# Kernel optimization log

Measured on AMD Instinct MI355X. Metric: run time of the kernel, lower is better.

## Reference

```python
import jax, jax.numpy as jnp
import numpy as np

# config (mirrors init_kwargs)
H = 768        # hidden_size
NH = 12        # n_heads
HD = H // NH   # head_size = 64 (rotary 'per_head' dim)
INTER = 3072   # intermediate_size
NL = 6         # n_layers
V = 32768      # vocab_size
AW = 256       # attention_width
SEQLEN = 512   # packed per-sequence length (batch['length'])
B = 16         # number of packed sequences
N = B * SEQLEN # total tokens


def _layer_norm(x, scale, offset, eps=1e-5):
    m = jnp.mean(x, axis=-1, keepdims=True)
    var = jnp.mean(jnp.square(x - m), axis=-1, keepdims=True)
    return (x - m) * jax.lax.rsqrt(var + eps) * scale + offset


def _rotate_every_two(x):
    x1 = x[..., ::2]
    x2 = x[..., 1::2]
    return jnp.stack((-x2, x1), axis=-1).reshape(x.shape)


def _fixed_pos_embedding(ages, dim):
    # ages: [N] float32 -> sin, cos: [N, dim]
    inv_freq = 1.0 / 10000 ** jnp.linspace(0.0, 2.0, num=dim // 2)
    t = ages[:, None] * inv_freq[None, :]          # [N, dim//2]
    s, c = jnp.sin(t), jnp.cos(t)
    sin = jnp.stack((s, s), axis=-1).reshape(ages.shape[0], dim)
    cos = jnp.stack((c, c), axis=-1).reshape(ages.shape[0], dim)
    return sin, cos


def _local_attention(q, k, v, seg_len, width):
    # q,k,v: [NH, N, HD]. Causal attention within a sliding window of `width`,
    # restricted to segments of size seg_len (the (i & ~(length-1)) mask in piton).
    nh, n, hd = q.shape
    b = n // seg_len
    qb = q.reshape(nh, b, seg_len, hd)
    kb = k.reshape(nh, b, seg_len, hd)
    vb = v.reshape(nh, b, seg_len, hd)
    scale = jnp.asarray(1.0 / np.sqrt(hd), q.dtype)
    scores = jnp.einsum('hbqd,hbkd->hbqk', qb, kb) * scale
    i = jnp.arange(seg_len)[:, None]
    j = jnp.arange(seg_len)[None, :]
    mask = (j <= i) & (i - j < width)
    scores = jnp.where(mask, scores, jnp.asarray(-1e30, scores.dtype))
    probs = jax.nn.softmax(scores, axis=-1)
    out = jnp.einsum('hbqk,hbkd->hbqd', probs, vb)
    return out.reshape(nh, n, hd)


def _block(x, sin, cos, seg_len, p):
    scale, offset, w_in, b_in, w_out, b_out = p
    xn = _layer_norm(x, scale, offset)
    mid = xn @ w_in + b_in                               # fused QKV + FF proj
    q, k, v, ff = jnp.split(mid, [H, 2 * H, 3 * H], axis=-1)

    def to_heads(t):  # [N, H] -> [NH, N, HD]
        return t.reshape(t.shape[0], NH, HD).transpose(1, 0, 2)

    q, k, v = to_heads(q), to_heads(k), to_heads(v)
    # rotary == 'per_head': applied after head split, sin/cos broadcast over heads
    q = q * cos[None] + _rotate_every_two(q) * sin[None]
    k = k * cos[None] + _rotate_every_two(k) * sin[None]
    attn = _local_attention(q, k, v, seg_len, AW)
    shaped = attn.transpose(1, 0, 2).reshape(x.shape)    # [N, H]
    combined = jnp.concatenate((shaped, jax.nn.gelu(ff)), axis=-1)
    # NOTE: original returns normed-x + output_proj(combined) (x was reassigned)
    return xn + combined @ w_out + b_out


def setup_inputs() -> dict:
    key = jax.random.key(0)
    ks = jax.random.split(key, 8)
    return {
        'tokens': jax.random.randint(ks[0], (N,), 0, V, dtype=jnp.int32),
        'ages': jax.random.uniform(ks[1], (N,), jnp.float32, 0.0, 10000.0),
        'normalized_ages': jax.random.normal(ks[2], (N,), jnp.float32),
        'length': SEQLEN,
        'embed': jax.random.normal(ks[3], (V, H), jnp.float32) / np.sqrt(H),
        'ln_scale': jnp.ones((NL, H), jnp.float32),
        'ln_offset': jnp.zeros((NL, H), jnp.float32),
        'w_in': jax.random.normal(ks[4], (NL, H, 3 * H + INTER), jnp.float32) / np.sqrt(H),
        'b_in': jnp.zeros((NL, 3 * H + INTER), jnp.float32),
        'w_out': jax.random.normal(ks[5], (NL, H + INTER, H), jnp.float32) * (2.0 / (NL * np.sqrt(H))),
        'b_out': jnp.zeros((NL, H), jnp.float32),
        'final_scale': jnp.ones((H,), jnp.float32),
        'final_offset': jnp.zeros((H,), jnp.float32),
    }


def reference(tokens, ages, normalized_ages, length, embed, ln_scale, ln_offset,
              w_in, b_in, w_out, b_out, final_scale, final_offset):
    x = embed[tokens]                                  # [N, H]
    sin, cos = _fixed_pos_embedding(ages, HD)          # rotary == 'per_head'

    def step(carry, p):
        return _block(carry, sin, cos, length, p), None

    x, _ = jax.lax.scan(step, x, (ln_scale, ln_offset, w_in, b_in, w_out, b_out))
    return _layer_norm(x, final_scale, final_offset)
```

## Files before the change

### kernel.cpp

```cpp
#include <hip/hip_runtime.h>
#include <hip/hip_bf16.h>

#define H_    768
#define NH_   12
#define HD_   64
#define INTER_ 3072
#define NL_   6
#define NTOK  8192
#define SEG   512
#define NB    16
#define AW_   256
#define MIDW  5376
#define CMB   3840

typedef unsigned short u16;
typedef __bf16 bf16;
typedef bf16  bf16x8 __attribute__((ext_vector_type(8)));
typedef float f32x4  __attribute__((ext_vector_type(4)));
typedef u16   u16x8  __attribute__((ext_vector_type(8)));

#define GLOAD16(gp, lp) \
    __builtin_amdgcn_global_load_lds((const __attribute__((address_space(1))) void*)(gp), \
                                     (__attribute__((address_space(3))) void*)(lp), 16, 0, 0)

__device__ __forceinline__ u16 f2bf(float f) {
    union { float f; unsigned u; } v; v.f = f;
    unsigned u = v.u;
    u += 0x7fffu + ((u >> 16) & 1u);
    return (u16)(u >> 16);
}
__device__ __forceinline__ float bf2f(u16 h) {
    union { unsigned u; float f; } v; v.u = ((unsigned)h) << 16; return v.f;
}
__device__ __forceinline__ float gelu_f(float x) {
    float x3 = x * x * x;
    return 0.5f * x * (1.f + tanhf(0.7978845608028654f * (x + 0.044715f * x3)));
}

__global__ void k_embed(const int* __restrict__ tokens, const float* __restrict__ embed,
                        float* __restrict__ x) {
    int row = blockIdx.x;
    int tok = tokens[row];
    const float* src = embed + (size_t)tok * H_;
    float* dst = x + (size_t)row * H_;
    for (int c = threadIdx.x; c < H_; c += blockDim.x) dst[c] = src[c];
}

__global__ void k_tables(const float* __restrict__ ages, float* __restrict__ st,
                         float* __restrict__ ct) {
    int n = blockIdx.x * blockDim.x + threadIdx.x;
    if (n >= NTOK) return;
    float age = ages[n];
    for (int j = 0; j < 32; j++) {
        float e = (float)j * (2.0f / 31.0f);
        float invf = 1.0f / powf(10000.0f, e);
        float t = age * invf;
        st[n * 32 + j] = sinf(t);
        ct[n * 32 + j] = cosf(t);
    }
}

__global__ void k_transpose_bf16(const float* __restrict__ src, u16* __restrict__ dst,
                                 int R, int C) {
    __shared__ float T[64][65];
    int l = blockIdx.z;
    const float* s = src + (size_t)l * R * C;
    u16* d = dst + (size_t)l * R * C;
    int r0 = blockIdx.y * 64, c0 = blockIdx.x * 64;
    for (int i = threadIdx.x; i < 64 * 64; i += blockDim.x) {
        int r = i >> 6, c = i & 63;
        T[r][c] = s[(size_t)(r0 + r) * C + c0 + c];
    }
    __syncthreads();
    for (int i = threadIdx.x; i < 64 * 64; i += blockDim.x) {
        int rr = i >> 6, cc = i & 63;
        d[(size_t)(c0 + rr) * R + r0 + cc] = f2bf(T[cc][rr]);
    }
}

template<int FINAL>
__global__ __launch_bounds__(256) void k_ln(const float* __restrict__ x,
        const float* __restrict__ scale, const float* __restrict__ offset,
        float* __restrict__ xn_f, u16* __restrict__ xn_h, float* __restrict__ outf) {
    int wid = threadIdx.x >> 6, lane = threadIdx.x & 63;
    int row = blockIdx.x * 4 + wid;
    const float* xr = x + (size_t)row * H_;
    float4 v[3];
    float s = 0.f, sq = 0.f;
#pragma unroll
    for (int i = 0; i < 3; i++) {
        v[i] = *(const float4*)&xr[(i * 64 + lane) * 4];
        s  += v[i].x + v[i].y + v[i].z + v[i].w;
        sq += v[i].x * v[i].x + v[i].y * v[i].y + v[i].z * v[i].z + v[i].w * v[i].w;
    }
    for (int m = 1; m < 64; m <<= 1) { s += __shfl_xor(s, m); sq += __shfl_xor(sq, m); }
    float mean = s * (1.f / 768.f);
    float var  = sq * (1.f / 768.f) - mean * mean;
    float rstd = rsqrtf(fmaxf(var, 0.f) + 1e-5f);
#pragma unroll
    for (int i = 0; i < 3; i++) {
        int c0 = (i * 64 + lane) * 4;
        float4 sc = *(const float4*)&scale[c0];
        float4 of = *(const float4*)&offset[c0];
        float y0 = (v[i].x - mean) * rstd * sc.x + of.x;
        float y1 = (v[i].y - mean) * rstd * sc.y + of.y;
        float y2 = (v[i].z - mean) * rstd * sc.z + of.z;
        float y3 = (v[i].w - mean) * rstd * sc.w + of.w;
        if (FINAL) {
            *(float4*)&outf[(size_t)row * H_ + c0] = make_float4(y0, y1, y2, y3);
        } else {
            *(float4*)&xn_f[(size_t)row * H_ + c0] = make_float4(y0, y1, y2, y3);
            ushort4 h = make_ushort4(f2bf(y0), f2bf(y1), f2bf(y2), f2bf(y3));
            *(ushort4*)&xn_h[(size_t)row * H_ + c0] = h;
        }
    }
}

template<int MODE, int BN>
__global__ __launch_bounds__(256) void k_gemm(
        const u16* __restrict__ A, const u16* __restrict__ A2,
        const u16* __restrict__ Bt, const float* __restrict__ bias,
        const float* __restrict__ xn_f, u16* __restrict__ Cmid,
        float* __restrict__ Xout, int Ksz) {
    __shared__ __align__(16) u16 As[128 * 64];
    __shared__ __align__(16) u16 Bs[BN * 64];
    int m0 = blockIdx.x * 128;
    int n0 = blockIdx.y * BN;
    int tid = threadIdx.x;
    int wid = tid >> 6, lane = tid & 63;
    constexpr int MI = (BN == 128) ? 4 : 2;
    constexpr int NI = 4;
    int wm = (BN == 128) ? (wid >> 1) : wid;
    int wn = (BN == 128) ? (wid & 1) : 0;
    f32x4 acc[MI][NI] = {};

    int r = tid >> 3;
    int cs = ((tid & 7) ^ ((tid >> 3) & 7)) * 8;
    int wbase = (tid & 192) * 8;

    int lm = lane & 15, lq = lane >> 4, l7 = lane & 7;

    int nkt = Ksz / 64;
    for (int kt = 0; kt < nkt; kt++) {
        int k0 = kt * 64;
        const u16* Ap; int lda, acol;
        if (MODE == 2 && k0 >= H_) { Ap = A2; lda = MIDW; acol = 2304 + (k0 - H_); }
        else                       { Ap = A;  lda = H_;   acol = k0; }
#pragma unroll
        for (int i = 0; i < 4; i++)
            GLOAD16(&Ap[(size_t)(m0 + i * 32 + r) * lda + acol + cs], &As[i * 2048 + wbase]);
#pragma unroll
        for (int i = 0; i < BN / 32; i++)
            GLOAD16(&Bt[(size_t)(n0 + i * 32 + r) * Ksz + k0 + cs], &Bs[i * 2048 + wbase]);
        __syncthreads();
#pragma unroll
        for (int kk = 0; kk < 64; kk += 32) {
            int slot = (((kk >> 3) + lq) ^ l7) * 8;
            bf16x8 af[MI], bfr[NI];
#pragma unroll
            for (int mi = 0; mi < MI; mi++)
                af[mi] = *(const bf16x8*)&As[(wm * (MI * 16) + mi * 16 + lm) * 64 + slot];
#pragma unroll
            for (int ni = 0; ni < NI; ni++)
                bfr[ni] = *(const bf16x8*)&Bs[(wn * 64 + ni * 16 + lm) * 64 + slot];
#pragma unroll
            for (int mi = 0; mi < MI; mi++)
#pragma unroll
                for (int ni = 0; ni < NI; ni++)
                    acc[mi][ni] = __builtin_amdgcn_mfma_f32_16x16x32_bf16(af[mi], bfr[ni], acc[mi][ni], 0, 0, 0);
        }
        __syncthreads();
    }
    int rbase = m0 + wm * (MI * 16), cbase = n0 + wn * 64;
#pragma unroll
    for (int mi = 0; mi < MI; mi++) {
#pragma unroll
        for (int ni = 0; ni < NI; ni++) {
            int col = cbase + ni * 16 + lm;
            float b = bias[col];
#pragma unroll
            for (int rr = 0; rr < 4; rr++) {
                int row = rbase + mi * 16 + lq * 4 + rr;
                float vv = acc[mi][ni][rr] + b;
                if (MODE == 1) {
                    if (col >= 2304) vv = gelu_f(vv);
                    Cmid[(size_t)row * MIDW + col] = f2bf(vv);
                } else {
                    Xout[(size_t)row * H_ + col] = vv + xn_f[(size_t)row * H_ + col];
                }
            }
        }
    }
}

__global__ __launch_bounds__(256) void k_rope_v(u16* __restrict__ mid,
        const float* __restrict__ st, const float* __restrict__ ct, u16* __restrict__ Vt) {
    int nb = blockIdx.x, h = blockIdx.y;
    int n0 = nb * 64;
    __shared__ u16 Vl[64][72];
    int tid = threadIdx.x;
    for (int i = tid; i < 64 * 32; i += 256) {
        int r = i >> 5, j = i & 31;
        int n = n0 + r;
        float s = st[n * 32 + j], c = ct[n * 32 + j];
        size_t base = (size_t)n * MIDW + h * 64 + 2 * j;
        float q0 = bf2f(mid[base]), q1 = bf2f(mid[base + 1]);
        mid[base]     = f2bf(q0 * c - q1 * s);
        mid[base + 1] = f2bf(q1 * c + q0 * s);
        float k0 = bf2f(mid[base + H_]), k1 = bf2f(mid[base + H_ + 1]);
        mid[base + H_]     = f2bf(k0 * c - k1 * s);
        mid[base + H_ + 1] = f2bf(k1 * c + k0 * s);
    }
    for (int i = tid; i < 64 * 64; i += 256) {
        int r = i >> 6, d = i & 63;
        Vl[r][d] = mid[(size_t)(n0 + r) * MIDW + 1536 + h * 64 + d];
    }
    __syncthreads();
    for (int i = tid; i < 64 * 64; i += 256) {
        int d = i >> 6, r = i & 63;
        Vt[(size_t)(h * 64 + d) * NTOK + n0 + r] = Vl[r][d];
    }
}

__global__ __launch_bounds__(128) void k_attn(const u16* __restrict__ mid,
        const u16* __restrict__ Vt, u16* __restrict__ attn_out) {
    int bx = blockIdx.x;
    int h = bx >> 8, rem = bx & 255, b = rem >> 4, qq = rem & 15;
    int t0 = (qq * 32 - 255) >> 6; if (t0 < 0) t0 = 0;
    int tend = qq >> 1;
    int nt = tend - t0 + 1;
    int tid = threadIdx.x, wid = tid >> 6, lane = tid & 63;
    __shared__ float S[32][324];
    __shared__ float rl[32];
    int qrow0 = b * SEG + qq * 32;

    bf16x8 qf[2];
    {
        int r = qrow0 + wid * 16 + (lane & 15);
        const u16* qp = &mid[(size_t)r * MIDW + h * 64];
        qf[0] = *(const bf16x8*)&qp[(lane >> 4) * 8];
        qf[1] = *(const bf16x8*)&qp[32 + (lane >> 4) * 8];
    }
    for (int t = 0; t < nt; t++) {
        int j0 = (t0 + t) * 64;
        f32x4 sa[4] = {};
#pragma unroll
        for (int kf = 0; kf < 2; kf++) {
            bf16x8 kfr[4];
#pragma unroll
            for (int nf = 0; nf < 4; nf++) {
                int key = b * SEG + j0 + nf * 16 + (lane & 15);
                kfr[nf] = *(const bf16x8*)&mid[(size_t)key * MIDW + H_ + h * 64 + kf * 32 + (lane >> 4) * 8];
            }
#pragma unroll
            for (int nf = 0; nf < 4; nf++)
                sa[nf] = __builtin_amdgcn_mfma_f32_16x16x32_bf16(qf[kf], kfr[nf], sa[nf], 0, 0, 0);
        }
#pragma unroll
        for (int nf = 0; nf < 4; nf++) {
            int j = j0 + nf * 16 + (lane & 15);
#pragma unroll
            for (int r = 0; r < 4; r++) {
                int row = wid * 16 + (lane >> 4) * 4 + r;
                int qi = qq * 32 + row;
                bool valid = (j <= qi) && (qi - j < AW_);
                S[row][t * 64 + nf * 16 + (lane & 15)] = valid ? sa[nf][r] * 0.125f : -1e30f;
            }
        }
    }
    __syncthreads();
    {
        int row = tid >> 2, sub = tid & 3;
        int ncol = nt * 64;
        float m = -1e30f;
        for (int c = sub; c < ncol; c += 4) m = fmaxf(m, S[row][c]);
        m = fmaxf(m, __shfl_xor(m, 1)); m = fmaxf(m, __shfl_xor(m, 2));
        float l = 0.f;
        for (int c = sub; c < ncol; c += 4) { float p = __expf(S[row][c] - m); S[row][c] = p; l += p; }
        l += __shfl_xor(l, 1); l += __shfl_xor(l, 2);
        if (sub == 0) rl[row] = 1.f / l;
    }
    __syncthreads();
    f32x4 oacc[4] = {};
    for (int t = 0; t < nt; t++) {
#pragma unroll
        for (int kf = 0; kf < 2; kf++) {
            const float* sp = &S[wid * 16 + (lane & 15)][t * 64 + kf * 32 + (lane >> 4) * 8];
            float4 f1 = *(const float4*)sp;
            float4 f2 = *(const float4*)(sp + 4);
            u16x8 pt;
            pt[0] = f2bf(f1.x); pt[1] = f2bf(f1.y); pt[2] = f2bf(f1.z); pt[3] = f2bf(f1.w);
            pt[4] = f2bf(f2.x); pt[5] = f2bf(f2.y); pt[6] = f2bf(f2.z); pt[7] = f2bf(f2.w);
            bf16x8 pa = __builtin_bit_cast(bf16x8, pt);
#pragma unroll
            for (int nf = 0; nf < 4; nf++) {
                int d = h * 64 + nf * 16 + (lane & 15);
                const u16* vp = &Vt[(size_t)d * NTOK + b * SEG + (t0 + t) * 64 + kf * 32 + (lane >> 4) * 8];
                bf16x8 vb = *(const bf16x8*)vp;
                oacc[nf] = __builtin_amdgcn_mfma_f32_16x16x32_bf16(pa, vb, oacc[nf], 0, 0, 0);
            }
        }
    }
#pragma unroll
    for (int nf = 0; nf < 4; nf++) {
#pragma unroll
        for (int r = 0; r < 4; r++) {
            int row = wid * 16 + (lane >> 4) * 4 + r;
            float sc = rl[row];
            int grow = qrow0 + row;
            attn_out[(size_t)grow * H_ + h * 64 + nf * 16 + (lane & 15)] = f2bf(oacc[nf][r] * sc);
        }
    }
}

extern "C" void kernel_launch(void* const* d_in, const int* in_sizes, int n_in,
                              void* d_out, int out_size, void* d_ws, size_t ws_size,
                              hipStream_t stream) {
    const int*   tokens   = (const int*)d_in[0];
    const float* ages     = (const float*)d_in[1];
    const float* embed    = (const float*)d_in[4];
    const float* ln_scale = (const float*)d_in[5];
    const float* ln_off   = (const float*)d_in[6];
    const float* w_in     = (const float*)d_in[7];
    const float* b_in     = (const float*)d_in[8];
    const float* w_out    = (const float*)d_in[9];
    const float* b_out    = (const float*)d_in[10];
    const float* fscale   = (const float*)d_in[11];
    const float* foff     = (const float*)d_in[12];
    float* out = (float*)d_out;

    char* ws = (char*)d_ws;
    size_t off = 0;
    auto alloc = [&](size_t bytes) { void* p = ws + off; off += (bytes + 255) & ~(size_t)255; return p; };
    float* st      = (float*)alloc((size_t)NTOK * 32 * 4);
    float* ct      = (float*)alloc((size_t)NTOK * 32 * 4);
    float* x       = (float*)alloc((size_t)NTOK * H_ * 4);
    float* xn_f    = (float*)alloc((size_t)NTOK * H_ * 4);
    u16*   xn_h    = (u16*)alloc((size_t)NTOK * H_ * 2);
    u16*   mid     = (u16*)alloc((size_t)NTOK * MIDW * 2);
    u16*   Vt      = (u16*)alloc((size_t)H_ * NTOK * 2);
    u16*   attn    = (u16*)alloc((size_t)NTOK * H_ * 2);
    u16*   w_in_t  = (u16*)alloc((size_t)NL_ * H_ * MIDW * 2);
    u16*   w_out_t = (u16*)alloc((size_t)NL_ * CMB * H_ * 2);

    k_embed<<<NTOK, 256, 0, stream>>>(tokens, embed, x);
    k_tables<<<(NTOK + 255) / 256, 256, 0, stream>>>(ages, st, ct);
    k_transpose_bf16<<<dim3(MIDW / 64, H_ / 64, NL_), 256, 0, stream>>>(w_in, w_in_t, H_, MIDW);
    k_transpose_bf16<<<dim3(H_ / 64, CMB / 64, NL_), 256, 0, stream>>>(w_out, w_out_t, CMB, H_);

    for (int l = 0; l < NL_; l++) {
        k_ln<0><<<NTOK / 4, 256, 0, stream>>>(x, ln_scale + l * H_, ln_off + l * H_, xn_f, xn_h, nullptr);
        k_gemm<1, 128><<<dim3(NTOK / 128, MIDW / 128), 256, 0, stream>>>(
            xn_h, nullptr, w_in_t + (size_t)l * H_ * MIDW, b_in + (size_t)l * MIDW,
            nullptr, mid, nullptr, H_);
        k_rope_v<<<dim3(NTOK / 64, NH_), 256, 0, stream>>>(mid, st, ct, Vt);
        k_attn<<<NH_ * NB * 16, 128, 0, stream>>>(mid, Vt, attn);
        k_gemm<2, 64><<<dim3(NTOK / 128, H_ / 64), 256, 0, stream>>>(
            attn, mid, w_out_t + (size_t)l * CMB * H_, b_out + (size_t)l * H_,
            xn_f, nullptr, x, CMB);
    }
    k_ln<1><<<NTOK / 4, 256, 0, stream>>>(x, fscale, foff, nullptr, nullptr, out);
}
```

Measured before the change: 2.077 ms.

## Replace QKV/FF GEMM with 256x256 eight-wave double-buffered pipelined kernel

The first projection GEMM now uses a 512-thread block computing 256x256 tiles, with double-buffered LDS, global-to-LDS prefetch of the next K tile spread across four compute phases, explicit vmcnt waits, raw barriers and setprio around the MFMA bursts. The tanh-based GELU is replaced with an algebraically equivalent exp form using fast intrinsics. The second GEMM is split into its own specialized kernel without template modes. The aim is more operand reuse per tile and overlap of memory loads with matrix math. In exchange the kernel uses 128 KB of LDS per block and needs many accumulator registers, which may limit occupancy.

```diff
diff --git a/kernel.cpp b/kernel.cpp
--- a/kernel.cpp
+++ b/kernel.cpp
@@ -23,6 +23,9 @@
     __builtin_amdgcn_global_load_lds((const __attribute__((address_space(1))) void*)(gp), \
                                      (__attribute__((address_space(3))) void*)(lp), 16, 0, 0)
 
+#define BAR() do { asm volatile("" ::: "memory"); __builtin_amdgcn_s_barrier(); \
+                   asm volatile("" ::: "memory"); } while (0)
+
 __device__ __forceinline__ u16 f2bf(float f) {
     union { float f; unsigned u; } v; v.f = f;
     unsigned u = v.u;
@@ -32,9 +35,11 @@
 __device__ __forceinline__ float bf2f(u16 h) {
     union { unsigned u; float f; } v; v.u = ((unsigned)h) << 16; return v.f;
 }
-__device__ __forceinline__ float gelu_f(float x) {
-    float x3 = x * x * x;
-    return 0.5f * x * (1.f + tanhf(0.7978845608028654f * (x + 0.044715f * x3)));
+__device__ __forceinline__ float gelu_fast(float x) {
+    float u = 1.5957691216057308f * x * (1.f + 0.044715f * x * x);
+    u = fminf(u, 80.f);
+    float e = __expf(u);
+    return __fdividef(x * e, e + 1.f);
 }
 
 __global__ void k_embed(const int* __restrict__ tokens, const float* __restrict__ embed,
@@ -116,78 +121,159 @@
     }
 }
 
-template<int MODE, int BN>
-__global__ __launch_bounds__(256) void k_gemm(
+__device__ __forceinline__ void stage_half(const u16* __restrict__ src, int row0,
+        int kc, u16* lds_half, int tid, int wid) {
+    int srow = tid >> 3;
+    int cs = ((tid & 7) ^ (srow & 7)) * 8;
+#pragma unroll
+    for (int rn = 0; rn < 2; rn++)
+        GLOAD16(&src[(size_t)(row0 + rn * 64 + srow) * H_ + kc + cs],
+                &lds_half[rn * 4096 + wid * 512]);
+}
+
+__global__ __launch_bounds__(512, 2) void k_gemm1_8p(
+        const u16* __restrict__ A, const u16* __restrict__ Bt,
+        const float* __restrict__ bias, u16* __restrict__ Cmid) {
+    __shared__ __align__(16) u16 As[2][2][128 * 64];
+    __shared__ __align__(16) u16 Bs[2][2][128 * 64];
+    const int m0 = blockIdx.x * 256;
+    const int n0 = blockIdx.y * 256;
+    const int tid = threadIdx.x;
+    const int wid = tid >> 6, lane = tid & 63;
+    const int wm = wid >> 2, wn = wid & 3;
+    const int lm = lane & 15, lq = lane >> 4, l7 = lane & 7;
+    f32x4 acc[8][4] = {};
+
+#pragma unroll
+    for (int h = 0; h < 2; h++) {
+        stage_half(A,  m0 + h * 128, 0, &As[0][h][0], tid, wid);
+        stage_half(Bt, n0 + h * 128, 0, &Bs[0][h][0], tid, wid);
+    }
+
+    const int NKT = H_ / 64;
+    for (int kt = 0; kt < NKT; kt++) {
+        const int cur = kt & 1, nxt = cur ^ 1;
+        const bool pf = (kt + 1 < NKT);
+        const int kc = (kt + 1) * 64;
+#pragma unroll
+        for (int q = 0; q < 4; q++) {
+            const int qm = q >> 1, qn = q & 1;
+            bf16x8 afr[2][4], bfr[2][2];
+            if (q == 0) {
+                if (pf) {
+                    stage_half(A, m0, kc, &As[nxt][0][0], tid, wid);
+                    asm volatile("s_waitcnt vmcnt(2)" ::: "memory");
+                } else {
+                    asm volatile("s_waitcnt vmcnt(0)" ::: "memory");
+                }
+                BAR();
+            }
+#pragma unroll
+            for (int kkk = 0; kkk < 2; kkk++) {
+                int slot = ((kkk * 4 + lq) ^ l7) * 8;
+#pragma unroll
+                for (int mi = 0; mi < 4; mi++)
+                    afr[kkk][mi] = *(const bf16x8*)&As[cur][wm][(qm * 64 + mi * 16 + lm) * 64 + slot];
+#pragma unroll
+                for (int ni = 0; ni < 2; ni++)
+                    bfr[kkk][ni] = *(const bf16x8*)&Bs[cur][wn >> 1][((wn & 1) * 64 + qn * 32 + ni * 16 + lm) * 64 + slot];
+            }
+            if (q == 1 && pf) stage_half(A,  m0 + 128, kc, &As[nxt][1][0], tid, wid);
+            if (q == 2 && pf) stage_half(Bt, n0,       kc, &Bs[nxt][0][0], tid, wid);
+            if (q == 3 && pf) stage_half(Bt, n0 + 128, kc, &Bs[nxt][1][0], tid, wid);
+            if (q != 0) BAR();
+            __builtin_amdgcn_s_setprio(1);
+#pragma unroll
+            for (int kkk = 0; kkk < 2; kkk++)
+#pragma unroll
+                for (int mi = 0; mi < 4; mi++)
+#pragma unroll
+                    for (int ni = 0; ni < 2; ni++)
+                        acc[qm * 4 + mi][qn * 2 + ni] =
+                            __builtin_amdgcn_mfma_f32_16x16x32_bf16(
+                                afr[kkk][mi], bfr[kkk][ni], acc[qm * 4 + mi][qn * 2 + ni], 0, 0, 0);
+            __builtin_amdgcn_s_setprio(0);
+            BAR();
+        }
+    }
+    const int rbase = m0 + wm * 128, cbase = n0 + wn * 64;
+#pragma unroll
+    for (int mi = 0; mi < 8; mi++) {
+#pragma unroll
+        for (int ni = 0; ni < 4; ni++) {
+            int col = cbase + ni * 16 + lm;
+            float b = bias[col];
+#pragma unroll
+            for (int rr = 0; rr < 4; rr++) {
+                int row = rbase + mi * 16 + lq * 4 + rr;
+                float vv = acc[mi][ni][rr] + b;
+                if (col >= 2304) vv = gelu_fast(vv);
+                Cmid[(size_t)row * MIDW + col] = f2bf(vv);
+            }
+        }
+    }
+}
+
+__global__ __launch_bounds__(256) void k_gemm2(
         const u16* __restrict__ A, const u16* __restrict__ A2,
         const u16* __restrict__ Bt, const float* __restrict__ bias,
-        const float* __restrict__ xn_f, u16* __restrict__ Cmid,
-        float* __restrict__ Xout, int Ksz) {
+        const float* __restrict__ xn_f, float* __restrict__ Xout, int Ksz) {
     __shared__ __align__(16) u16 As[128 * 64];
-    __shared__ __align__(16) u16 Bs[BN * 64];
+    __shared__ __align__(16) u16 Bs[64 * 64];
     int m0 = blockIdx.x * 128;
-    int n0 = blockIdx.y * BN;
+    int n0 = blockIdx.y * 64;
     int tid = threadIdx.x;
     int wid = tid >> 6, lane = tid & 63;
-    constexpr int MI = (BN == 128) ? 4 : 2;
-    constexpr int NI = 4;
-    int wm = (BN == 128) ? (wid >> 1) : wid;
-    int wn = (BN == 128) ? (wid & 1) : 0;
-    f32x4 acc[MI][NI] = {};
+    int wm = wid, wn = 0;
+    f32x4 acc[2][4] = {};
 
     int r = tid >> 3;
     int cs = ((tid & 7) ^ ((tid >> 3) & 7)) * 8;
     int wbase = (tid & 192) * 8;
-
     int lm = lane & 15, lq = lane >> 4, l7 = lane & 7;
 
     int nkt = Ksz / 64;
     for (int kt = 0; kt < nkt; kt++) {
         int k0 = kt * 64;
         const u16* Ap; int lda, acol;
-        if (MODE == 2 && k0 >= H_) { Ap = A2; lda = MIDW; acol = 2304 + (k0 - H_); }
-        else                       { Ap = A;  lda = H_;   acol = k0; }
+        if (k0 >= H_) { Ap = A2; lda = MIDW; acol = 2304 + (k0 - H_); }
+        else          { Ap = A;  lda = H_;   acol = k0; }
 #pragma unroll
         for (int i = 0; i < 4; i++)
             GLOAD16(&Ap[(size_t)(m0 + i * 32 + r) * lda + acol + cs], &As[i * 2048 + wbase]);
 #pragma unroll
-        for (int i = 0; i < BN / 32; i++)
+        for (int i = 0; i < 2; i++)
             GLOAD16(&Bt[(size_t)(n0 + i * 32 + r) * Ksz + k0 + cs], &Bs[i * 2048 + wbase]);
         __syncthreads();
 #pragma unroll
         for (int kk = 0; kk < 64; kk += 32) {
             int slot = (((kk >> 3) + lq) ^ l7) * 8;
-            bf16x8 af[MI], bfr[NI];
-#pragma unroll
-            for (int mi = 0; mi < MI; mi++)
-                af[mi] = *(const bf16x8*)&As[(wm * (MI * 16) + mi * 16 + lm) * 64 + slot];
-#pragma unroll
-            for (int ni = 0; ni < NI; ni++)
-                bfr[ni] = *(const bf16x8*)&Bs[(wn * 64 + ni * 16 + lm) * 64 + slot];
-#pragma unroll
-            for (int mi = 0; mi < MI; mi++)
-#pragma unroll
-                for (int ni = 0; ni < NI; ni++)
+            bf16x8 af[2], bfr[4];
+#pragma unroll
+            for (int mi = 0; mi < 2; mi++)
+                af[mi] = *(const bf16x8*)&As[(wm * 32 + mi * 16 + lm) * 64 + slot];
+#pragma unroll
+            for (int ni = 0; ni < 4; ni++)
+                bfr[ni] = *(const bf16x8*)&Bs[(ni * 16 + lm) * 64 + slot];
+#pragma unroll
+            for (int mi = 0; mi < 2; mi++)
+#pragma unroll
+                for (int ni = 0; ni < 4; ni++)
                     acc[mi][ni] = __builtin_amdgcn_mfma_f32_16x16x32_bf16(af[mi], bfr[ni], acc[mi][ni], 0, 0, 0);
         }
         __syncthreads();
     }
-    int rbase = m0 + wm * (MI * 16), cbase = n0 + wn * 64;
-#pragma unroll
-    for (int mi = 0; mi < MI; mi++) {
-#pragma unroll
-        for (int ni = 0; ni < NI; ni++) {
+    int rbase = m0 + wm * 32, cbase = n0;
+#pragma unroll
+    for (int mi = 0; mi < 2; mi++) {
+#pragma unroll
+        for (int ni = 0; ni < 4; ni++) {
             int col = cbase + ni * 16 + lm;
             float b = bias[col];
 #pragma unroll
             for (int rr = 0; rr < 4; rr++) {
                 int row = rbase + mi * 16 + lq * 4 + rr;
-                float vv = acc[mi][ni][rr] + b;
-                if (MODE == 1) {
-                    if (col >= 2304) vv = gelu_f(vv);
-                    Cmid[(size_t)row * MIDW + col] = f2bf(vv);
-                } else {
-                    Xout[(size_t)row * H_ + col] = vv + xn_f[(size_t)row * H_ + col];
-                }
+                Xout[(size_t)row * H_ + col] = acc[mi][ni][rr] + b + xn_f[(size_t)row * H_ + col];
             }
         }
     }
@@ -350,14 +436,13 @@
 
     for (int l = 0; l < NL_; l++) {
         k_ln<0><<<NTOK / 4, 256, 0, stream>>>(x, ln_scale + l * H_, ln_off + l * H_, xn_f, xn_h, nullptr);
-        k_gemm<1, 128><<<dim3(NTOK / 128, MIDW / 128), 256, 0, stream>>>(
-            xn_h, nullptr, w_in_t + (size_t)l * H_ * MIDW, b_in + (size_t)l * MIDW,
-            nullptr, mid, nullptr, H_);
+        k_gemm1_8p<<<dim3(NTOK / 256, MIDW / 256), 512, 0, stream>>>(
+            xn_h, w_in_t + (size_t)l * H_ * MIDW, b_in + (size_t)l * MIDW, mid);
         k_rope_v<<<dim3(NTOK / 64, NH_), 256, 0, stream>>>(mid, st, ct, Vt);
         k_attn<<<NH_ * NB * 16, 128, 0, stream>>>(mid, Vt, attn);
-        k_gemm<2, 64><<<dim3(NTOK / 128, H_ / 64), 256, 0, stream>>>(
+        k_gemm2<<<dim3(NTOK / 128, H_ / 64), 256, 0, stream>>>(
             attn, mid, w_out_t + (size_t)l * CMB * H_, b_out + (size_t)l * H_,
-            xn_f, nullptr, x, CMB);
+            xn_f, x, CMB);
     }
     k_ln<1><<<NTOK / 4, 256, 0, stream>>>(x, fscale, foff, nullptr, nullptr, out);
 }
```

Result: no change. 2.102 ms (+1.2%).
